# Kernel tuning notes

Measured on AMD Instinct MI355X. Metric: run time of the kernel, lower is better.

## Reference

```python
import jax, jax.numpy as jnp
import numpy as np

MAX_HOP = 3

def setup_inputs() -> dict:
    key = jax.random.key(0)
    k1, k2, k3 = jax.random.split(key, 3)
    B, M, D = 8, 8192, 256
    query_vector = jax.random.normal(k1, (B, D), dtype=jnp.float32)
    global_pointer = jax.random.uniform(k2, (B, M), dtype=jnp.float32)  # sigmoid-range
    m_story = jax.random.normal(k3, (MAX_HOP + 1, B, M, D), dtype=jnp.float32) * 0.1
    return {"query_vector": query_vector, "global_pointer": global_pointer, "m_story": m_story}


def reference(query_vector, global_pointer, m_story):
    # query_vector: [B, D]; global_pointer: [B, M]; m_story: [H+1, B, M, D]
    u = query_vector
    gp = global_pointer[:, :, None]  # [B, M, 1]
    prob_soft = None
    prob_logits = None
    for hop in range(MAX_HOP):
        m_A = m_story[hop] * gp                       # [B, M, D] pointer gating
        prob_logits = jnp.einsum('bmd,bd->bm', m_A, u)  # broadcast mul + sum over D
        prob_soft = jax.nn.softmax(prob_logits, axis=1)  # softmax over memory dim
        m_C = m_story[hop + 1] * gp                   # [B, M, D]
        o_k = jnp.einsum('bm,bmd->bd', prob_soft, m_C)  # weighted sum over memory
        u = u + o_k
    return (prob_soft, prob_logits)
```

## Files before the change

kernel.cpp:

```cpp
#include <hip/hip_runtime.h>
#include <hip/hip_bf16.h>

#define B 8
#define M 8192
#define D 256
#define BM (B * M)
#define BMD ((size_t)B * M * D)

__global__ __launch_bounds__(256) void hop_kernel(
    const float* __restrict__ st_h,
    const float* __restrict__ st_next,
    const float* __restrict__ query,
    const float* __restrict__ gp,
    const float* __restrict__ on0, const float* __restrict__ z0,
    const float* __restrict__ on1, const float* __restrict__ z1,
    float* __restrict__ onum_out,
    float* __restrict__ z_out,
    float* __restrict__ logits_out,
    float* __restrict__ psum_out)
{
    const int bid = blockIdx.x;
    const int b = bid >> 7;
    const int tid = threadIdx.x, lane = tid & 63, wv = tid >> 6;
    const long long grow0 = (long long)bid * 64;

    __shared__ float uu[256];
    __shared__ float gpv[64];
    __shared__ float w[64];
    __shared__ float sred[4];
    __shared__ float sacc[4][256];

    float uq = query[b * 256 + tid];
    if (on0) uq += on0[b * 256 + tid] / z0[b];
    if (on1) uq += on1[b * 256 + tid] / z1[b];
    uu[tid] = uq;
    if (tid < 64) gpv[tid] = gp[grow0 + tid];
    __syncthreads();

    const float4 uf = reinterpret_cast<const float4*>(uu)[lane];

    const float4* s1 = reinterpret_cast<const float4*>(st_h + grow0 * D) + lane;
    float esum = 0.f;
    #pragma unroll
    for (int r = 0; r < 16; ++r) {
        const int row = (wv << 4) + r;
        float4 s = s1[(size_t)row * 64];
        float v = s.x * uf.x + s.y * uf.y + s.z * uf.z + s.w * uf.w;
        #pragma unroll
        for (int off = 32; off; off >>= 1) v += __shfl_xor(v, off, 64);
        if (lane == 0) {
            const float g = gpv[row];
            const float l = v * g;
            const float e = __expf(l);
            esum += e;
            w[row] = e * g;
            if (logits_out) logits_out[grow0 + row] = l;
        }
    }
    if (lane == 0) sred[wv] = esum;
    __syncthreads();

    if (st_next == nullptr) {
        if (tid == 0) psum_out[bid] = sred[0] + sred[1] + sred[2] + sred[3];
        return;
    }

    const float4* s2 = reinterpret_cast<const float4*>(st_next + grow0 * D) + lane;
    float4 acc = {0.f, 0.f, 0.f, 0.f};
    #pragma unroll
    for (int r = 0; r < 16; ++r) {
        const int row = (wv << 4) + r;
        float4 s = s2[(size_t)row * 64];
        const float ww = w[row];
        acc.x += ww * s.x; acc.y += ww * s.y; acc.z += ww * s.z; acc.w += ww * s.w;
    }
    reinterpret_cast<float4*>(&sacc[wv][0])[lane] = acc;
    __syncthreads();
    const float o = sacc[0][tid] + sacc[1][tid] + sacc[2][tid] + sacc[3][tid];
    atomicAdd(&onum_out[b * 256 + tid], o);
    if (tid == 0) atomicAdd(z_out + b, sred[0] + sred[1] + sred[2] + sred[3]);
}

__global__ __launch_bounds__(256) void prob_kernel(
    const float* __restrict__ logits,
    const float* __restrict__ psum,
    float* __restrict__ prob)
{
    const int tid = threadIdx.x;
    const int b = blockIdx.x >> 5;
    __shared__ float red[128];
    if (tid < 128) red[tid] = psum[b * 128 + tid];
    __syncthreads();
    for (int s = 64; s; s >>= 1) {
        if (tid < s) red[tid] += red[tid + s];
        __syncthreads();
    }
    const float inv = 1.f / red[0];
    const int i = blockIdx.x * 256 + tid;
    prob[i] = __expf(logits[i]) * inv;
}

extern "C" void kernel_launch(void* const* d_in, const int* in_sizes, int n_in,
                              void* d_out, int out_size, void* d_ws, size_t ws_size,
                              hipStream_t stream) {
    const float* query = (const float*)d_in[0];
    const float* gp    = (const float*)d_in[1];
    const float* story = (const float*)d_in[2];

    float* out    = (float*)d_out;
    float* prob   = out;
    float* logits = out + BM;

    float* ws   = (float*)d_ws;
    float* on0  = ws;
    float* z0   = ws + 2048;
    float* on1  = ws + 2048 + 8;
    float* z1   = ws + 4096 + 8;
    float* psum = ws + 4104;

    const float* st0 = story;
    const float* st1 = story + BMD;
    const float* st2 = story + 2 * BMD;

    hipMemsetAsync(ws, 0, 4112 * sizeof(float), stream);

    hop_kernel<<<BM / 64, 256, 0, stream>>>(st0, st1, query, gp,
                                            nullptr, nullptr, nullptr, nullptr,
                                            on0, z0, nullptr, nullptr);
    hop_kernel<<<BM / 64, 256, 0, stream>>>(st1, st2, query, gp,
                                            on0, z0, nullptr, nullptr,
                                            on1, z1, nullptr, nullptr);
    hop_kernel<<<BM / 64, 256, 0, stream>>>(st2, nullptr, query, gp,
                                            on0, z0, on1, z1,
                                            nullptr, nullptr, logits, psum);
    prob_kernel<<<BM / 256, 256, 0, stream>>>(logits, psum, prob);
}
```

Measured before the change: 86.16 us.

## Fuse all hops and softmax into one persistent kernel with grid barriers

Replaces the three per-hop kernel launches and the separate probability kernel with a single persistent kernel of 256 blocks of 1024 threads. Hops are synchronised with atomic-counter grid barriers. Each block keeps the same 256 memory rows across hops, so a story slab read in one hop's weighted sum is read again by the same block in the next hop's dot product, which may be served from cache. This removes launch gaps and the extra logits re-read, but it relies on all blocks being co-resident and adds spin-wait barrier cost, with only one large block per CU.

```diff
diff --git a/kernel.cpp b/kernel.cpp
--- a/kernel.cpp
+++ b/kernel.cpp
@@ -1,103 +1,144 @@
 #include <hip/hip_runtime.h>
-#include <hip/hip_bf16.h>
 
 #define B 8
 #define M 8192
 #define D 256
 #define BM (B * M)
 #define BMD ((size_t)B * M * D)
+#define NBLK 256
+#define NTHR 1024
+#define RPB 256
+#define NWV 16
 
-__global__ __launch_bounds__(256) void hop_kernel(
-    const float* __restrict__ st_h,
-    const float* __restrict__ st_next,
+__device__ __forceinline__ void grid_barrier(unsigned* cnt) {
+    __syncthreads();
+    if (threadIdx.x == 0) {
+        __hip_atomic_fetch_add(cnt, 1u, __ATOMIC_ACQ_REL, __HIP_MEMORY_SCOPE_AGENT);
+        while (__hip_atomic_load(cnt, __ATOMIC_ACQUIRE, __HIP_MEMORY_SCOPE_AGENT)
+               < (unsigned)NBLK)
+            __builtin_amdgcn_s_sleep(2);
+    }
+    __syncthreads();
+}
+
+__global__ __launch_bounds__(NTHR) void multihop_kernel(
+    const float* __restrict__ story,
     const float* __restrict__ query,
     const float* __restrict__ gp,
-    const float* __restrict__ on0, const float* __restrict__ z0,
-    const float* __restrict__ on1, const float* __restrict__ z1,
-    float* __restrict__ onum_out,
-    float* __restrict__ z_out,
-    float* __restrict__ logits_out,
-    float* __restrict__ psum_out)
+    float* __restrict__ prob,
+    float* __restrict__ logits,
+    unsigned* __restrict__ cnt,
+    float* __restrict__ on0,
+    float* __restrict__ on1,
+    float* __restrict__ psum)
 {
     const int bid = blockIdx.x;
-    const int b = bid >> 7;
+    const int b = bid >> 5;
     const int tid = threadIdx.x, lane = tid & 63, wv = tid >> 6;
-    const long long grow0 = (long long)bid * 64;
+    const long long grow0 = (long long)bid * RPB;
 
     __shared__ float uu[256];
-    __shared__ float gpv[64];
-    __shared__ float w[64];
-    __shared__ float sred[4];
-    __shared__ float sacc[4][256];
+    __shared__ float gpv[RPB];
+    __shared__ float w[RPB];
+    __shared__ float l2s[RPB];
+    __shared__ float sred[NWV];
+    __shared__ float sacc[NWV][256];
+    __shared__ float zsh;
 
-    float uq = query[b * 256 + tid];
-    if (on0) uq += on0[b * 256 + tid] / z0[b];
-    if (on1) uq += on1[b * 256 + tid] / z1[b];
-    uu[tid] = uq;
-    if (tid < 64) gpv[tid] = gp[grow0 + tid];
+    const float* st0 = story;
+    const float* st1 = story + BMD;
+    const float* st2 = story + 2 * BMD;
+
+    if (tid < RPB) gpv[tid] = gp[grow0 + tid];
+    const float qv = (tid < 256) ? query[b * 256 + tid] : 0.f;
+
+    auto dot_phase = [&](const float* st, int slot, bool final_hop) {
+        const float4 uf = reinterpret_cast<const float4*>(uu)[lane];
+        const float4* s4 = reinterpret_cast<const float4*>(st + grow0 * D) + lane;
+        float esum = 0.f;
+        #pragma unroll
+        for (int r = 0; r < 16; ++r) {
+            const int lr = (wv << 4) + r;
+            float4 s = s4[(size_t)lr * 64];
+            float v = s.x * uf.x + s.y * uf.y + s.z * uf.z + s.w * uf.w;
+            #pragma unroll
+            for (int off = 32; off; off >>= 1) v += __shfl_xor(v, off, 64);
+            if (lane == 0) {
+                const float g = gpv[lr];
+                const float l = v * g;
+                const float e = __expf(l);
+                esum += e;
+                w[lr] = e * g;
+                if (final_hop) { logits[grow0 + lr] = l; l2s[lr] = l; }
+            }
+        }
+        if (lane == 0) sred[wv] = esum;
+        __syncthreads();
+        if (tid == 0) {
+            float z = 0.f;
+            #pragma unroll
+            for (int k = 0; k < NWV; ++k) z += sred[k];
+            psum[slot * NBLK + bid] = z;
+        }
+        __syncthreads();
+    };
+
+    auto o_phase = [&](const float* st, float* onum) {
+        const float4* s4 = reinterpret_cast<const float4*>(st + grow0 * D) + lane;
+        float4 acc = {0.f, 0.f, 0.f, 0.f};
+        #pragma unroll
+        for (int r = 0; r < 16; ++r) {
+            const int lr = (wv << 4) + r;
+            float4 s = s4[(size_t)lr * 64];
+            const float ww = w[lr];
+            acc.x += ww * s.x; acc.y += ww * s.y; acc.z += ww * s.z; acc.w += ww * s.w;
+        }
+        reinterpret_cast<float4*>(&sacc[wv][0])[lane] = acc;
+        __syncthreads();
+        if (tid < 256) {
+            float s = 0.f;
+            #pragma unroll
+            for (int k = 0; k < NWV; ++k) s += sacc[k][tid];
+            atomicAdd(&onum[b * 256 + tid], s);
+        }
+        __syncthreads();
+    };
+
+    auto zsum = [&](int slot) -> float {
+        if (tid < 32) {
+            float v = psum[slot * NBLK + b * 32 + tid];
+            #pragma unroll
+            for (int off = 16; off; off >>= 1) v += __shfl_xor(v, off, 64);
+            if (tid == 0) zsh = v;
+        }
+        __syncthreads();
+        return zsh;
+    };
+
+    if (tid < 256) uu[tid] = qv;
     __syncthreads();
+    dot_phase(st0, 0, false);
 
-    const float4 uf = reinterpret_cast<const float4*>(uu)[lane];
+    o_phase(st1, on0);
+    grid_barrier(cnt + 0);
 
-    const float4* s1 = reinterpret_cast<const float4*>(st_h + grow0 * D) + lane;
-    float esum = 0.f;
-    #pragma unroll
-    for (int r = 0; r < 16; ++r) {
-        const int row = (wv << 4) + r;
-        float4 s = s1[(size_t)row * 64];
-        float v = s.x * uf.x + s.y * uf.y + s.z * uf.z + s.w * uf.w;
-        #pragma unroll
-        for (int off = 32; off; off >>= 1) v += __shfl_xor(v, off, 64);
-        if (lane == 0) {
-            const float g = gpv[row];
-            const float l = v * g;
-            const float e = __expf(l);
-            esum += e;
-            w[row] = e * g;
-            if (logits_out) logits_out[grow0 + row] = l;
-        }
-    }
-    if (lane == 0) sred[wv] = esum;
+    const float z0 = zsum(0);
+    float f0 = 0.f;
+    if (tid < 256) { f0 = on0[b * 256 + tid] / z0; uu[tid] = qv + f0; }
     __syncthreads();
+    dot_phase(st1, 1, false);
 
-    if (st_next == nullptr) {
-        if (tid == 0) psum_out[bid] = sred[0] + sred[1] + sred[2] + sred[3];
-        return;
-    }
+    o_phase(st2, on1);
+    grid_barrier(cnt + 16);
 
-    const float4* s2 = reinterpret_cast<const float4*>(st_next + grow0 * D) + lane;
-    float4 acc = {0.f, 0.f, 0.f, 0.f};
-    #pragma unroll
-    for (int r = 0; r < 16; ++r) {
-        const int row = (wv << 4) + r;
-        float4 s = s2[(size_t)row * 64];
-        const float ww = w[row];
-        acc.x += ww * s.x; acc.y += ww * s.y; acc.z += ww * s.z; acc.w += ww * s.w;
-    }
-    reinterpret_cast<float4*>(&sacc[wv][0])[lane] = acc;
+    const float z1 = zsum(1);
+    if (tid < 256) uu[tid] = qv + f0 + on1[b * 256 + tid] / z1;
     __syncthreads();
-    const float o = sacc[0][tid] + sacc[1][tid] + sacc[2][tid] + sacc[3][tid];
-    atomicAdd(&onum_out[b * 256 + tid], o);
-    if (tid == 0) atomicAdd(z_out + b, sred[0] + sred[1] + sred[2] + sred[3]);
-}
+    dot_phase(st2, 2, true);
+    grid_barrier(cnt + 32);
 
-__global__ __launch_bounds__(256) void prob_kernel(
-    const float* __restrict__ logits,
-    const float* __restrict__ psum,
-    float* __restrict__ prob)
-{
-    const int tid = threadIdx.x;
-    const int b = blockIdx.x >> 5;
-    __shared__ float red[128];
-    if (tid < 128) red[tid] = psum[b * 128 + tid];
-    __syncthreads();
-    for (int s = 64; s; s >>= 1) {
-        if (tid < s) red[tid] += red[tid + s];
-        __syncthreads();
-    }
-    const float inv = 1.f / red[0];
-    const int i = blockIdx.x * 256 + tid;
-    prob[i] = __expf(logits[i]) * inv;
+    const float z2 = zsum(2);
+    if (tid < 256) prob[grow0 + tid] = __expf(l2s[tid]) / z2;
 }
 
 extern "C" void kernel_launch(void* const* d_in, const int* in_sizes, int n_in,
@@ -111,27 +152,14 @@
     float* prob   = out;
     float* logits = out + BM;
 
-    float* ws   = (float*)d_ws;
-    float* on0  = ws;
-    float* z0   = ws + 2048;
-    float* on1  = ws + 2048 + 8;
-    float* z1   = ws + 4096 + 8;
-    float* psum = ws + 4104;
+    float* ws = (float*)d_ws;
+    unsigned* cnt = (unsigned*)ws;
+    float* on0  = ws + 256;
+    float* on1  = ws + 256 + 2048;
+    float* psum = ws + 256 + 4096;
 
-    const float* st0 = story;
-    const float* st1 = story + BMD;
-    const float* st2 = story + 2 * BMD;
+    hipMemsetAsync(ws, 0, (256 + 4096) * sizeof(float), stream);
 
-    hipMemsetAsync(ws, 0, 4112 * sizeof(float), stream);
-
-    hop_kernel<<<BM / 64, 256, 0, stream>>>(st0, st1, query, gp,
-                                            nullptr, nullptr, nullptr, nullptr,
-                                            on0, z0, nullptr, nullptr);
-    hop_kernel<<<BM / 64, 256, 0, stream>>>(st1, st2, query, gp,
-                                            on0, z0, nullptr, nullptr,
-                                            on1, z1, nullptr, nullptr);
-    hop_kernel<<<BM / 64, 256, 0, stream>>>(st2, nullptr, query, gp,
-                                            on0, z0, on1, z1,
-                                            nullptr, nullptr, logits, psum);
-    prob_kernel<<<BM / 256, 256, 0, stream>>>(logits, psum, prob);
+    multihop_kernel<<<NBLK, NTHR, 0, stream>>>(story, query, gp, prob, logits,
+                                               cnt, on0, on1, psum);
 }
```

Measured after the change: 147.5 us. 1.71x slower.
